# Kernel tuning notes

Hardware: AMD Instinct MI355X
Metric: run time of the kernel (lower is better)

The kernel has to match this reference:

```python
import jax, jax.numpy as jnp
import numpy as np


def _ln(x, w, b):
    m = x.mean(-1, keepdims=True)
    v = ((x - m) ** 2).mean(-1, keepdims=True)
    return (x - m) / jnp.sqrt(v + 1e-5) * w + b


def setup_inputs() -> dict:
    key = jax.random.key(0)
    ks = jax.random.split(key, 8)
    N, C, H, W = 2, 64, 128, 128
    heads, ksz = 2, 7
    C4 = 4 * C
    p = lambda k, shape: jax.random.normal(k, shape, dtype=jnp.float32) * 0.02
    return {
        "x": jax.random.normal(ks[0], (N, C, H, W), dtype=jnp.float32),
        "qkv_w": p(ks[1], (3 * C, C)),
        "qkv_b": jnp.zeros((3 * C,), jnp.float32),
        "proj_w": p(ks[2], (C, C)),
        "proj_b": jnp.zeros((C,), jnp.float32),
        "rpb": p(ks[3], (heads, 2 * ksz - 1, 2 * ksz - 1)),
        "ln1_w": jnp.ones((C,), jnp.float32),
        "ln1_b": jnp.zeros((C,), jnp.float32),
        "ln2_w": jnp.ones((C,), jnp.float32),
        "ln2_b": jnp.zeros((C,), jnp.float32),
        "fc1_w": p(ks[4], (C4, C)),
        "fc1_b": jnp.zeros((C4,), jnp.float32),
        "fc2_w": p(ks[5], (C, C4)),
        "fc2_b": jnp.zeros((C,), jnp.float32),
    }


def reference(x, qkv_w, qkv_b, proj_w, proj_b, rpb, ln1_w, ln1_b, ln2_w, ln2_b,
              fc1_w, fc1_b, fc2_w, fc2_b):
    N, C, H, W = x.shape
    heads = rpb.shape[0]
    ksz = (rpb.shape[1] + 1) // 2  # kernel size from (2k-1) bias table
    dh = C // heads

    xt = x.transpose(0, 2, 3, 1).reshape(N, H * W, C)  # n (h w) c
    shortcut = xt
    xn = _ln(xt, ln1_w, ln1_b).reshape(N, H, W, C)

    # qkv projection -> (3, N, heads, H, W, dh)
    qkv = (xn @ qkv_w.T + qkv_b).reshape(N, H, W, 3, heads, dh)
    qkv = qkv.transpose(3, 0, 4, 1, 2, 5)
    q = qkv[0] * (dh ** -0.5)
    k = qkv[1]
    v = qkv[2]

    # NATTEN neighborhood: window start clamped so every query sees k x k keys
    sh = jnp.clip(jnp.arange(H) - ksz // 2, 0, H - ksz)
    sw = jnp.clip(jnp.arange(W) - ksz // 2, 0, W - ksz)
    rows = sh[:, None] + jnp.arange(ksz)  # (H, k) key row indices
    cols = sw[:, None] + jnp.arange(ksz)  # (W, k) key col indices

    # relative position bias index: (query - key) + (k-1) in [0, 2k-2]
    rel_h = jnp.arange(H)[:, None] - rows + (ksz - 1)  # (H, k)
    rel_w = jnp.arange(W)[:, None] - cols + (ksz - 1)  # (W, k)
    bias = rpb[:, rel_h][:, :, :, rel_w]               # (heads, H, k, W, k)
    bias = bias.transpose(0, 1, 3, 2, 4)               # (heads, H, W, k, k)

    ri = rows[:, None, :, None]  # (H,1,k,1)
    ci = cols[None, :, None, :]  # (1,W,1,k)
    kwin = k[:, :, ri, ci, :]    # (N, heads, H, W, k, k, dh)
    vwin = v[:, :, ri, ci, :]

    scores = jnp.einsum('nzhwd,nzhwijd->nzhwij', q, kwin) + bias[None]
    attn = jax.nn.softmax(scores.reshape(N, heads, H, W, ksz * ksz), axis=-1)
    out = jnp.einsum('nzhwe,nzhwed->nzhwd', attn,
                     vwin.reshape(N, heads, H, W, ksz * ksz, dh))
    out = out.transpose(0, 2, 3, 1, 4).reshape(N, H, W, C) @ proj_w.T + proj_b

    x2 = shortcut + out.reshape(N, H * W, C)
    y = _ln(x2, ln2_w, ln2_b)
    y = jax.nn.gelu(y @ fc1_w.T + fc1_b, approximate=False) @ fc2_w.T + fc2_b
    x3 = x2 + y
    return x3.reshape(N, H, W, C).transpose(0, 3, 1, 2)
```

## Files before the change

kernel.cpp:

```cpp
#include <hip/hip_runtime.h>
#include <math.h>

#define TQ   32768
#define HWSZ 16384
#define CC   64
#define HH   128
#define WW   128
#define C3   192
#define C4   256
#define KS   7

typedef _Float16 half2v __attribute__((ext_vector_type(2)));
typedef _Float16 half4v __attribute__((ext_vector_type(4)));
typedef _Float16 half8v __attribute__((ext_vector_type(8)));
typedef float    f32x4  __attribute__((ext_vector_type(4)));

#define MFMA16(a, b, c) __builtin_amdgcn_mfma_f32_16x16x32_f16((a), (b), (c), 0, 0, 0)

__device__ __forceinline__ float gelu_f(float v) {
    float z = v * (1.59576912f + 0.07135481f * v * v);
    float e = __expf(-z);
    return v * (1.f / (1.f + e));
}

__global__ __launch_bounds__(256) void k_qkvln(const float* __restrict__ x,
        const float* __restrict__ lnw, const float* __restrict__ lnb,
        const float* __restrict__ qw, const float* __restrict__ qb,
        const float* __restrict__ pw, const float* __restrict__ f1w,
        const float* __restrict__ f2w,
        _Float16* __restrict__ qkv16, _Float16* __restrict__ pw16,
        _Float16* __restrict__ f1w16, _Float16* __restrict__ f2w16) {
    __shared__ union {
        struct { __align__(16) _Float16 A[64 * 72]; __align__(16) _Float16 B[192 * 72]; } st;
        __align__(16) _Float16 outb[64 * 200];
    } u;
    __shared__ float ps1[256], ps2[256], m_s[64], r_s[64];
    __shared__ float w_s[64], b_s[64], bias_s[192];
    int tid = threadIdx.x;
    int t0 = blockIdx.x * 64;
    if (tid < 64) { w_s[tid] = lnw[tid]; b_s[tid] = lnb[tid]; }
    if (tid < 192) bias_s[tid] = qb[tid];
    int tok = tid & 63, cq = tid >> 6;
    int t = t0 + tok;
    int n = t >> 14, hw = t & (HWSZ - 1);
    const float* xr = x + ((size_t)n << 20) + hw;
    float v[16];
    float s = 0.f, s2 = 0.f;
#pragma unroll
    for (int e = 0; e < 16; ++e) {
        float f = xr[(cq * 16 + e) * HWSZ];
        v[e] = f; s += f; s2 += f * f;
    }
    ps1[tid] = s; ps2[tid] = s2;
    for (int i = tid; i < 3072; i += 256) {
        int jj = i >> 4, seg = i & 15;
        float4 v4 = *(const float4*)&qw[(size_t)jj * 64 + seg * 4];
        half4v h4 = { (_Float16)v4.x, (_Float16)v4.y, (_Float16)v4.z, (_Float16)v4.w };
        *(half4v*)&u.st.B[jj * 72 + seg * 4] = h4;
    }
    {
        int g = blockIdx.x * 256 + tid;
        if (g < 4096) pw16[g] = (_Float16)pw[g];
        else if (g < 20480) f1w16[g - 4096] = (_Float16)f1w[g - 4096];
        else if (g < 36864) f2w16[g - 20480] = (_Float16)f2w[g - 20480];
    }
    __syncthreads();
    if (tid < 64) {
        float ss = ps1[tid] + ps1[tid + 64] + ps1[tid + 128] + ps1[tid + 192];
        float qq = ps2[tid] + ps2[tid + 64] + ps2[tid + 128] + ps2[tid + 192];
        float m = ss * (1.f / 64.f);
        float var = qq * (1.f / 64.f) - m * m;
        m_s[tid] = m; r_s[tid] = rsqrtf(var + 1e-5f);
    }
    __syncthreads();
    {
        float m = m_s[tok], r = r_s[tok];
#pragma unroll
        for (int u8 = 0; u8 < 2; ++u8) {
            half8v o;
#pragma unroll
            for (int e = 0; e < 8; ++e) {
                int c = cq * 16 + u8 * 8 + e;
                o[e] = (_Float16)((v[u8 * 8 + e] - m) * r * w_s[c] + b_s[c]);
            }
            *(half8v*)&u.st.A[tok * 72 + cq * 16 + u8 * 8] = o;
        }
    }
    __syncthreads();
    int lane = tid & 63, wv = tid >> 6;
    int quad = lane >> 4, l16 = lane & 15;
    int nt0 = wv * 48;
    f32x4 acc[4][3];
#pragma unroll
    for (int mf = 0; mf < 4; ++mf)
#pragma unroll
        for (int nf = 0; nf < 3; ++nf) acc[mf][nf] = (f32x4){0.f, 0.f, 0.f, 0.f};
#pragma unroll
    for (int ks = 0; ks < 64; ks += 32) {
        half8v a[4], bfr[3];
#pragma unroll
        for (int mf = 0; mf < 4; ++mf)
            a[mf] = *(const half8v*)&u.st.A[(mf * 16 + l16) * 72 + ks + quad * 8];
#pragma unroll
        for (int nf = 0; nf < 3; ++nf)
            bfr[nf] = *(const half8v*)&u.st.B[(nt0 + nf * 16 + l16) * 72 + ks + quad * 8];
#pragma unroll
        for (int mf = 0; mf < 4; ++mf)
#pragma unroll
            for (int nf = 0; nf < 3; ++nf) acc[mf][nf] = MFMA16(a[mf], bfr[nf], acc[mf][nf]);
    }
    __syncthreads();
    const float qscale = 0.17677669529663687f;
#pragma unroll
    for (int mf = 0; mf < 4; ++mf)
#pragma unroll
        for (int nf = 0; nf < 3; ++nf) {
            int j = nt0 + nf * 16 + l16;
            float bias = bias_s[j];
            float sc = (j < 64) ? qscale : 1.f;
#pragma unroll
            for (int r = 0; r < 4; ++r) {
                int tl = mf * 16 + quad * 4 + r;
                u.outb[tl * 200 + j] = (_Float16)((acc[mf][nf][r] + bias) * sc);
            }
        }
    __syncthreads();
    for (int i = tid; i < 2048; i += 256) {
        int tk = i >> 5, rem = i & 31;
        if (rem < 24)
            *(half8v*)&qkv16[(size_t)(t0 + tk) * C3 + rem * 8] =
                *(const half8v*)&u.outb[tk * 200 + rem * 8];
    }
}

__global__ __launch_bounds__(256) void k_attn_mlp(const _Float16* __restrict__ qkv16,
        const float* __restrict__ rpb,
        const _Float16* __restrict__ pw16, const float* __restrict__ pb,
        const float* __restrict__ x,
        const float* __restrict__ ln2w, const float* __restrict__ ln2b,
        const _Float16* __restrict__ f1w16, const float* __restrict__ f1b,
        const _Float16* __restrict__ f2w16, const float* __restrict__ f2b,
        float* __restrict__ out) {
    __shared__ __align__(16) char smem[78216];
    _Float16* kv_s  = (_Float16*)smem;
    _Float16* q_s   = (_Float16*)(smem + 53312);
    _Float16* s_s   = (_Float16*)(smem + 63552);
    float*    rpb_s = (float*)(smem + 76352);
    float*    sum_s = (float*)(smem + 77704);
    float* x2t  = (float*)smem;
    float* ps1  = (float*)(smem + 20480);
    float* ps2  = (float*)(smem + 21504);
    float* m_s  = (float*)(smem + 22528);
    float* r_s  = (float*)(smem + 22784);
    float* w_s  = (float*)(smem + 23040);
    float* b_s  = (float*)(smem + 23296);
    float* pb_s = (float*)(smem + 23552);
    _Float16* A2_s = (_Float16*)(smem + 53312);
    _Float16* H_s  = (_Float16*)(smem + 17408);
    float*    tr_s = (float*)(smem + 17408);
    float*    f1b_s = (float*)(smem + 63552);
    float*    f2b_s = (float*)(smem + 64576);

    int tid = threadIdx.x;
    int bx = blockIdx.x;
    int n  = bx >> 8;
    int th = (bx >> 4) & 15, tw = bx & 15;
    int h0 = th * 8, w0 = tw * 8;
    int wr0 = min(max(h0 - 3, 0), HH - 14);
    int ww0 = min(max(w0 - 3, 0), WW - 14);
    int tbase = n << 14;
    int lane = tid & 63, wvi = tid >> 6;
    int quad = lane >> 4, l16 = lane & 15;

    for (int i = tid; i < 338; i += 256) rpb_s[i] = rpb[i];
    for (int i = tid; i < 196 * 16; i += 256) {
        int tok = i >> 4, u = i & 15;
        int wi = tok / 14, wj = tok - wi * 14;
        *(half8v*)&kv_s[tok * 136 + u * 8] = *(const half8v*)&qkv16[
            (size_t)(tbase + (wr0 + wi) * WW + ww0 + wj) * C3 + 64 + u * 8];
    }
    for (int i = tid; i < 64 * 8; i += 256) {
        int q = i >> 3, u = i & 7;
        int qg = tbase + (h0 + (q >> 3)) * WW + (w0 + (q & 7));
        *(half8v*)&q_s[q * 80 + u * 8] = *(const half8v*)&qkv16[(size_t)qg * C3 + u * 8];
    }
    half8v pwr0 = *(const half8v*)&pw16[(size_t)tid * 8];
    half8v pwr1 = *(const half8v*)&pw16[(size_t)(tid + 256) * 8];
    __syncthreads();

    int c16 = tid & 1, z = (tid >> 1) & 1, q = tid >> 2;
    int qy = q >> 3, qx = q & 7;
    int h = h0 + qy, wc = w0 + qx;
    int sh = min(max(h - 3, 0), HH - KS);
    int sw = min(max(wc - 3, 0), WW - KS);
    int oh = sh - wr0, ow = sw - ww0;
    int dhp = h - sh + 6, dwp = wc - sw + 6;
    {
        const half8v* qp = (const half8v*)&q_s[q * 80 + z * 32];
        half8v q0 = qp[0], q1 = qp[1], q2 = qp[2], q3 = qp[3];
        int i7 = 0, j7 = c16;
        for (int nb = c16; nb < 49; nb += 2) {
            int tok = (oh + i7) * 14 + (ow + j7);
            const half8v* kp = (const half8v*)&kv_s[tok * 136 + z * 32];
            half2v acc2 = { (_Float16)0.f, (_Float16)0.f };
            half8v k0 = kp[0], k1 = kp[1], k2 = kp[2], k3 = kp[3];
            acc2 += (half2v){k0.s0, k0.s1} * (half2v){q0.s0, q0.s1};
            acc2 += (half2v){k0.s2, k0.s3} * (half2v){q0.s2, q0.s3};
            acc2 += (half2v){k0.s4, k0.s5} * (half2v){q0.s4, q0.s5};
            acc2 += (half2v){k0.s6, k0.s7} * (half2v){q0.s6, q0.s7};
            acc2 += (half2v){k1.s0, k1.s1} * (half2v){q1.s0, q1.s1};
            acc2 += (half2v){k1.s2, k1.s3} * (half2v){q1.s2, q1.s3};
            acc2 += (half2v){k1.s4, k1.s5} * (half2v){q1.s4, q1.s5};
            acc2 += (half2v){k1.s6, k1.s7} * (half2v){q1.s6, q1.s7};
            acc2 += (half2v){k2.s0, k2.s1} * (half2v){q2.s0, q2.s1};
            acc2 += (half2v){k2.s2, k2.s3} * (half2v){q2.s2, q2.s3};
            acc2 += (half2v){k2.s4, k2.s5} * (half2v){q2.s4, q2.s5};
            acc2 += (half2v){k2.s6, k2.s7} * (half2v){q2.s6, q2.s7};
            acc2 += (half2v){k3.s0, k3.s1} * (half2v){q3.s0, q3.s1};
            acc2 += (half2v){k3.s2, k3.s3} * (half2v){q3.s2, q3.s3};
            acc2 += (half2v){k3.s4, k3.s5} * (half2v){q3.s4, q3.s5};
            acc2 += (half2v){k3.s6, k3.s7} * (half2v){q3.s6, q3.s7};
            float s = (float)acc2.x + (float)acc2.y
                    + rpb_s[(z * 13 + (dhp - i7)) * 13 + (dwp - j7)];
            s_s[(q * 2 + z) * 50 + nb] = (_Float16)s;
            j7 += 2;
            if (j7 >= 7) { j7 -= 7; ++i7; }
        }
    }
    __syncthreads();

    {
        int row = tid >> 1, h2 = tid & 1;
        _Float16* sp = &s_s[row * 50];
        int i0 = h2 ? 25 : 0, i1 = h2 ? 49 : 25;
        float mx = -1e30f;
        for (int i = i0; i < i1; ++i) mx = fmaxf(mx, (float)sp[i]);
        mx = fmaxf(mx, __shfl_xor(mx, 1));
        float sum = 0.f;
        for (int i = i0; i < i1; ++i) {
            float e = __expf((float)sp[i] - mx);
            sum += e;
            sp[i] = (_Float16)e;
        }
        sum += __shfl_xor(sum, 1);
        if (h2 == 0) sum_s[row] = 1.f / sum;
    }
    __syncthreads();

    {
        const _Float16* pp = &s_s[(q * 2 + z) * 50];
        half2v acc[8];
#pragma unroll
        for (int j = 0; j < 8; ++j) acc[j] = (half2v){ (_Float16)0.f, (_Float16)0.f };
        int i7 = 0, j7 = 0;
        for (int nb = 0; nb < 49; ++nb) {
            int tok = (oh + i7) * 14 + (ow + j7);
            _Float16 p = pp[nb];
            half2v p2 = { p, p };
            const half8v* vp = (const half8v*)&kv_s[tok * 136 + 64 + z * 32 + c16 * 16];
            half8v v0 = vp[0], v1 = vp[1];
            acc[0] += (half2v){v0.s0, v0.s1} * p2;
            acc[1] += (half2v){v0.s2, v0.s3} * p2;
            acc[2] += (half2v){v0.s4, v0.s5} * p2;
            acc[3] += (half2v){v0.s6, v0.s7} * p2;
            acc[4] += (half2v){v1.s0, v1.s1} * p2;
            acc[5] += (half2v){v1.s2, v1.s3} * p2;
            acc[6] += (half2v){v1.s4, v1.s5} * p2;
            acc[7] += (half2v){v1.s6, v1.s7} * p2;
            ++j7;
            if (j7 == 7) { j7 = 0; ++i7; }
        }
        float inv = sum_s[q * 2 + z];
        _Float16* op = q_s + q * 72 + z * 32 + c16 * 16;
        half8v o0, o1;
#pragma unroll
        for (int j = 0; j < 4; ++j) {
            o0[2 * j]     = (_Float16)((float)acc[j].x * inv);
            o0[2 * j + 1] = (_Float16)((float)acc[j].y * inv);
            o1[2 * j]     = (_Float16)((float)acc[4 + j].x * inv);
            o1[2 * j + 1] = (_Float16)((float)acc[4 + j].y * inv);
        }
        *(half8v*)op = o0;
        *(half8v*)(op + 8) = o1;
    }
    __syncthreads();
    {
        int i0 = tid, i1 = tid + 256;
        *(half8v*)&s_s[(i0 >> 3) * 72 + (i0 & 7) * 8] = pwr0;
        *(half8v*)&s_s[(i1 >> 3) * 72 + (i1 & 7) * 8] = pwr1;
    }
    if (tid < 64) { w_s[tid] = ln2w[tid]; b_s[tid] = ln2b[tid]; pb_s[tid] = pb[tid]; }
    __syncthreads();
    {
        int mt0 = wvi * 16;
        f32x4 acc2[4];
#pragma unroll
        for (int nf = 0; nf < 4; ++nf) acc2[nf] = (f32x4){0.f, 0.f, 0.f, 0.f};
#pragma unroll
        for (int ks = 0; ks < 64; ks += 32) {
            half8v a = *(const half8v*)&q_s[(mt0 + l16) * 72 + ks + quad * 8];
            half8v bfr[4];
#pragma unroll
            for (int nf = 0; nf < 4; ++nf)
                bfr[nf] = *(const half8v*)&s_s[(nf * 16 + l16) * 72 + ks + quad * 8];
#pragma unroll
            for (int nf = 0; nf < 4; ++nf) acc2[nf] = MFMA16(a, bfr[nf], acc2[nf]);
        }
        __syncthreads();
        int tl0 = mt0 + quad * 4;
        int hwl = (h0 + (tl0 >> 3)) * WW + w0 + (tl0 & 7);
#pragma unroll
        for (int nf = 0; nf < 4; ++nf) {
            int j = nf * 16 + l16;
            float bias = pb_s[j];
            float4 rx = *(const float4*)&x[((size_t)(n * CC + j) << 14) + hwl];
#pragma unroll
            for (int r = 0; r < 4; ++r)
                x2t[(tl0 + r) * 68 + j] = acc2[nf][r] + bias + ((const float*)&rx)[r];
        }
    }
    f1b_s[tid] = f1b[tid];
    if (tid < 64) f2b_s[tid] = f2b[tid];
    __syncthreads();
    int tok = tid & 63, cq = tid >> 6;
    {
        float s = 0.f, s2 = 0.f;
#pragma unroll
        for (int e = 0; e < 16; ++e) {
            float f = x2t[tok * 68 + cq * 16 + e];
            s += f; s2 += f * f;
        }
        ps1[tid] = s; ps2[tid] = s2;
    }
    __syncthreads();
    if (tid < 64) {
        float ss = ps1[tid] + ps1[64 + tid] + ps1[128 + tid] + ps1[192 + tid];
        float qq = ps2[tid] + ps2[64 + tid] + ps2[128 + tid] + ps2[192 + tid];
        float m = ss * (1.f / 64.f);
        float var = qq * (1.f / 64.f) - m * m;
        m_s[tid] = m; r_s[tid] = rsqrtf(var + 1e-5f);
    }
    __syncthreads();
    {
        float m = m_s[tok], r = r_s[tok];
        half8v nv0, nv1;
#pragma unroll
        for (int e = 0; e < 8; ++e) {
            int c = cq * 16 + e;
            float f = x2t[tok * 68 + c];
            nv0[e] = (_Float16)((f - m) * r * w_s[c] + b_s[c]);
        }
#pragma unroll
        for (int e = 0; e < 8; ++e) {
            int c = cq * 16 + 8 + e;
            float f = x2t[tok * 68 + c];
            nv1[e] = (_Float16)((f - m) * r * w_s[c] + b_s[c]);
        }
        *(half8v*)&A2_s[tok * 72 + cq * 16] = nv0;
        *(half8v*)&A2_s[tok * 72 + cq * 16 + 8] = nv1;
    }
    __syncthreads();
    {
        int nt0 = wvi * 64;
        f32x4 acc[4][4];
#pragma unroll
        for (int mf = 0; mf < 4; ++mf)
#pragma unroll
            for (int nf = 0; nf < 4; ++nf) acc[mf][nf] = (f32x4){0.f, 0.f, 0.f, 0.f};
#pragma unroll
        for (int ks = 0; ks < 64; ks += 32) {
            half8v a[4], bfr[4];
#pragma unroll
            for (int mf = 0; mf < 4; ++mf)
                a[mf] = *(const half8v*)&A2_s[(mf * 16 + l16) * 72 + ks + quad * 8];
#pragma unroll
            for (int nf = 0; nf < 4; ++nf)
                bfr[nf] = *(const half8v*)&f1w16[(size_t)(nt0 + nf * 16 + l16) * 64 + ks + quad * 8];
#pragma unroll
            for (int mf = 0; mf < 4; ++mf)
#pragma unroll
                for (int nf = 0; nf < 4; ++nf) acc[mf][nf] = MFMA16(a[mf], bfr[nf], acc[mf][nf]);
        }
#pragma unroll
        for (int mf = 0; mf < 4; ++mf)
#pragma unroll
            for (int nf = 0; nf < 4; ++nf) {
                int jl = nt0 + nf * 16 + l16;
                float bias = f1b_s[jl];
#pragma unroll
                for (int r = 0; r < 4; ++r) {
                    int tl = mf * 16 + quad * 4 + r;
                    H_s[tl * 264 + jl] = (_Float16)gelu_f(acc[mf][nf][r] + bias);
                }
            }
    }
    __syncthreads();
    {
        int mt = wvi * 16;
        f32x4 acc2[4];
#pragma unroll
        for (int nf = 0; nf < 4; ++nf) acc2[nf] = (f32x4){0.f, 0.f, 0.f, 0.f};
#pragma unroll
        for (int ks = 0; ks < 256; ks += 32) {
            half8v a = *(const half8v*)&H_s[(mt + l16) * 264 + ks + quad * 8];
            half8v bfr[4];
#pragma unroll
            for (int nf = 0; nf < 4; ++nf)
                bfr[nf] = *(const half8v*)&f2w16[(size_t)(nf * 16 + l16) * 256 + ks + quad * 8];
#pragma unroll
            for (int nf = 0; nf < 4; ++nf) acc2[nf] = MFMA16(a, bfr[nf], acc2[nf]);
        }
        __syncthreads();
#pragma unroll
        for (int nf = 0; nf < 4; ++nf) {
            int j = nf * 16 + l16;
            float bias = f2b_s[j];
#pragma unroll
            for (int r = 0; r < 4; ++r) {
                int tl = mt + quad * 4 + r;
                float v = acc2[nf][r] + bias + x2t[tl * 68 + j];
                tr_s[j * 68 + tl] = v;
            }
        }
    }
    __syncthreads();
    for (int i = tid; i < 2048; i += 256) {
        int j = i >> 5, tl = (i & 31) * 2;
        *(float2*)&out[((size_t)(n * CC + j) << 14)
                       + (size_t)((h0 + (tl >> 3)) * WW + w0 + (tl & 7))] =
            *(const float2*)&tr_s[j * 68 + tl];
    }
}

extern "C" void kernel_launch(void* const* d_in, const int* in_sizes, int n_in,
                              void* d_out, int out_size, void* d_ws, size_t ws_size,
                              hipStream_t stream) {
    const float* x      = (const float*)d_in[0];
    const float* qkv_w  = (const float*)d_in[1];
    const float* qkv_b  = (const float*)d_in[2];
    const float* proj_w = (const float*)d_in[3];
    const float* proj_b = (const float*)d_in[4];
    const float* rpb    = (const float*)d_in[5];
    const float* ln1_w  = (const float*)d_in[6];
    const float* ln1_b  = (const float*)d_in[7];
    const float* ln2_w  = (const float*)d_in[8];
    const float* ln2_b  = (const float*)d_in[9];
    const float* fc1_w  = (const float*)d_in[10];
    const float* fc1_b  = (const float*)d_in[11];
    const float* fc2_w  = (const float*)d_in[12];
    const float* fc2_b  = (const float*)d_in[13];
    float* out = (float*)d_out;
    char* ws = (char*)d_ws;

    _Float16* qkv16  = (_Float16*)(ws);
    _Float16* pw16   = (_Float16*)(ws + 20971520);
    _Float16* f1w16  = (_Float16*)(ws + 20979712);
    _Float16* f2w16  = (_Float16*)(ws + 21012480);

    k_qkvln   <<<512, 256, 0, stream>>>(x, ln1_w, ln1_b, qkv_w, qkv_b,
                                        proj_w, fc1_w, fc2_w,
                                        qkv16, pw16, f1w16, f2w16);
    k_attn_mlp<<<512, 256, 0, stream>>>(qkv16, rpb, pw16, proj_b, x, ln2_w, ln2_b,
                                        f1w16, fc1_b, f2w16, fc2_b, out);
}
```

Measured before the change: 127.8 us.

## Fuse LN1+QKV projection into attention kernel, recomputing halo tokens per tile

Removes the separate LN1/QKV kernel and its fp16 qkv workspace round-trip. Each 8x8 tile block now loads the 14x14 halo of x directly, applies LayerNorm, and runs the QKV MFMA GEMM in four 49-token chunks, writing K/V and the in-tile Q straight into shared memory. Weights are converted from fp32 to fp16 on the fly instead of being pre-converted. The trade is recomputing QKV for about three times as many tokens as needed (the halo overlap), plus redundant weight conversion in every block, in exchange for one fewer launch and less global traffic.

```diff
diff --git a/kernel.cpp b/kernel.cpp
--- a/kernel.cpp
+++ b/kernel.cpp
@@ -1,13 +1,10 @@
 #include <hip/hip_runtime.h>
 #include <math.h>
 
-#define TQ   32768
 #define HWSZ 16384
 #define CC   64
 #define HH   128
 #define WW   128
-#define C3   192
-#define C4   256
 #define KS   7
 
 typedef _Float16 half2v __attribute__((ext_vector_type(2)));
@@ -23,123 +20,21 @@
     return v * (1.f / (1.f + e));
 }
 
-__global__ __launch_bounds__(256) void k_qkvln(const float* __restrict__ x,
-        const float* __restrict__ lnw, const float* __restrict__ lnb,
-        const float* __restrict__ qw, const float* __restrict__ qb,
-        const float* __restrict__ pw, const float* __restrict__ f1w,
-        const float* __restrict__ f2w,
-        _Float16* __restrict__ qkv16, _Float16* __restrict__ pw16,
-        _Float16* __restrict__ f1w16, _Float16* __restrict__ f2w16) {
-    __shared__ union {
-        struct { __align__(16) _Float16 A[64 * 72]; __align__(16) _Float16 B[192 * 72]; } st;
-        __align__(16) _Float16 outb[64 * 200];
-    } u;
-    __shared__ float ps1[256], ps2[256], m_s[64], r_s[64];
-    __shared__ float w_s[64], b_s[64], bias_s[192];
-    int tid = threadIdx.x;
-    int t0 = blockIdx.x * 64;
-    if (tid < 64) { w_s[tid] = lnw[tid]; b_s[tid] = lnb[tid]; }
-    if (tid < 192) bias_s[tid] = qb[tid];
-    int tok = tid & 63, cq = tid >> 6;
-    int t = t0 + tok;
-    int n = t >> 14, hw = t & (HWSZ - 1);
-    const float* xr = x + ((size_t)n << 20) + hw;
-    float v[16];
-    float s = 0.f, s2 = 0.f;
-#pragma unroll
-    for (int e = 0; e < 16; ++e) {
-        float f = xr[(cq * 16 + e) * HWSZ];
-        v[e] = f; s += f; s2 += f * f;
-    }
-    ps1[tid] = s; ps2[tid] = s2;
-    for (int i = tid; i < 3072; i += 256) {
-        int jj = i >> 4, seg = i & 15;
-        float4 v4 = *(const float4*)&qw[(size_t)jj * 64 + seg * 4];
-        half4v h4 = { (_Float16)v4.x, (_Float16)v4.y, (_Float16)v4.z, (_Float16)v4.w };
-        *(half4v*)&u.st.B[jj * 72 + seg * 4] = h4;
-    }
-    {
-        int g = blockIdx.x * 256 + tid;
-        if (g < 4096) pw16[g] = (_Float16)pw[g];
-        else if (g < 20480) f1w16[g - 4096] = (_Float16)f1w[g - 4096];
-        else if (g < 36864) f2w16[g - 20480] = (_Float16)f2w[g - 20480];
-    }
-    __syncthreads();
-    if (tid < 64) {
-        float ss = ps1[tid] + ps1[tid + 64] + ps1[tid + 128] + ps1[tid + 192];
-        float qq = ps2[tid] + ps2[tid + 64] + ps2[tid + 128] + ps2[tid + 192];
-        float m = ss * (1.f / 64.f);
-        float var = qq * (1.f / 64.f) - m * m;
-        m_s[tid] = m; r_s[tid] = rsqrtf(var + 1e-5f);
-    }
-    __syncthreads();
-    {
-        float m = m_s[tok], r = r_s[tok];
-#pragma unroll
-        for (int u8 = 0; u8 < 2; ++u8) {
-            half8v o;
-#pragma unroll
-            for (int e = 0; e < 8; ++e) {
-                int c = cq * 16 + u8 * 8 + e;
-                o[e] = (_Float16)((v[u8 * 8 + e] - m) * r * w_s[c] + b_s[c]);
-            }
-            *(half8v*)&u.st.A[tok * 72 + cq * 16 + u8 * 8] = o;
-        }
-    }
-    __syncthreads();
-    int lane = tid & 63, wv = tid >> 6;
-    int quad = lane >> 4, l16 = lane & 15;
-    int nt0 = wv * 48;
-    f32x4 acc[4][3];
-#pragma unroll
-    for (int mf = 0; mf < 4; ++mf)
-#pragma unroll
-        for (int nf = 0; nf < 3; ++nf) acc[mf][nf] = (f32x4){0.f, 0.f, 0.f, 0.f};
-#pragma unroll
-    for (int ks = 0; ks < 64; ks += 32) {
-        half8v a[4], bfr[3];
-#pragma unroll
-        for (int mf = 0; mf < 4; ++mf)
-            a[mf] = *(const half8v*)&u.st.A[(mf * 16 + l16) * 72 + ks + quad * 8];
-#pragma unroll
-        for (int nf = 0; nf < 3; ++nf)
-            bfr[nf] = *(const half8v*)&u.st.B[(nt0 + nf * 16 + l16) * 72 + ks + quad * 8];
-#pragma unroll
-        for (int mf = 0; mf < 4; ++mf)
-#pragma unroll
-            for (int nf = 0; nf < 3; ++nf) acc[mf][nf] = MFMA16(a[mf], bfr[nf], acc[mf][nf]);
-    }
-    __syncthreads();
-    const float qscale = 0.17677669529663687f;
-#pragma unroll
-    for (int mf = 0; mf < 4; ++mf)
-#pragma unroll
-        for (int nf = 0; nf < 3; ++nf) {
-            int j = nt0 + nf * 16 + l16;
-            float bias = bias_s[j];
-            float sc = (j < 64) ? qscale : 1.f;
-#pragma unroll
-            for (int r = 0; r < 4; ++r) {
-                int tl = mf * 16 + quad * 4 + r;
-                u.outb[tl * 200 + j] = (_Float16)((acc[mf][nf][r] + bias) * sc);
-            }
-        }
-    __syncthreads();
-    for (int i = tid; i < 2048; i += 256) {
-        int tk = i >> 5, rem = i & 31;
-        if (rem < 24)
-            *(half8v*)&qkv16[(size_t)(t0 + tk) * C3 + rem * 8] =
-                *(const half8v*)&u.outb[tk * 200 + rem * 8];
-    }
+__device__ __forceinline__ half8v cvt8(const float* p) {
+    float4 a0 = *(const float4*)p, a1 = *(const float4*)(p + 4);
+    return (half8v){(_Float16)a0.x, (_Float16)a0.y, (_Float16)a0.z, (_Float16)a0.w,
+                    (_Float16)a1.x, (_Float16)a1.y, (_Float16)a1.z, (_Float16)a1.w};
 }
 
-__global__ __launch_bounds__(256) void k_attn_mlp(const _Float16* __restrict__ qkv16,
+__global__ __launch_bounds__(256) void k_block(
+        const float* __restrict__ x,
+        const float* __restrict__ qw,  const float* __restrict__ qb,
+        const float* __restrict__ pw,  const float* __restrict__ pb,
         const float* __restrict__ rpb,
-        const _Float16* __restrict__ pw16, const float* __restrict__ pb,
-        const float* __restrict__ x,
+        const float* __restrict__ ln1w, const float* __restrict__ ln1b,
         const float* __restrict__ ln2w, const float* __restrict__ ln2b,
-        const _Float16* __restrict__ f1w16, const float* __restrict__ f1b,
-        const _Float16* __restrict__ f2w16, const float* __restrict__ f2b,
+        const float* __restrict__ f1w, const float* __restrict__ f1b,
+        const float* __restrict__ f2w, const float* __restrict__ f2b,
         float* __restrict__ out) {
     __shared__ __align__(16) char smem[78216];
     _Float16* kv_s  = (_Float16*)smem;
@@ -147,6 +42,12 @@
     _Float16* s_s   = (_Float16*)(smem + 63552);
     float*    rpb_s = (float*)(smem + 76352);
     float*    sum_s = (float*)(smem + 77704);
+    _Float16* A_s   = (_Float16*)(smem + 63552);
+    float* ps1c  = (float*)(smem + 72768);
+    float* ps2c  = (float*)(smem + 73184);
+    float* lnw_s = (float*)(smem + 73600);
+    float* lnb_s = (float*)(smem + 73856);
+    float* qb_s  = (float*)(smem + 74112);
     float* x2t  = (float*)smem;
     float* ps1  = (float*)(smem + 20480);
     float* ps2  = (float*)(smem + 21504);
@@ -168,24 +69,112 @@
     int h0 = th * 8, w0 = tw * 8;
     int wr0 = min(max(h0 - 3, 0), HH - 14);
     int ww0 = min(max(w0 - 3, 0), WW - 14);
-    int tbase = n << 14;
     int lane = tid & 63, wvi = tid >> 6;
     int quad = lane >> 4, l16 = lane & 15;
 
+    if (tid < 64) { lnw_s[tid] = ln1w[tid]; lnb_s[tid] = ln1b[tid]; }
+    if (tid < 192) qb_s[tid] = qb[tid];
     for (int i = tid; i < 338; i += 256) rpb_s[i] = rpb[i];
-    for (int i = tid; i < 196 * 16; i += 256) {
-        int tok = i >> 4, u = i & 15;
-        int wi = tok / 14, wj = tok - wi * 14;
-        *(half8v*)&kv_s[tok * 136 + u * 8] = *(const half8v*)&qkv16[
-            (size_t)(tbase + (wr0 + wi) * WW + ww0 + wj) * C3 + 64 + u * 8];
-    }
-    for (int i = tid; i < 64 * 8; i += 256) {
-        int q = i >> 3, u = i & 7;
-        int qg = tbase + (h0 + (q >> 3)) * WW + (w0 + (q & 7));
-        *(half8v*)&q_s[q * 80 + u * 8] = *(const half8v*)&qkv16[(size_t)qg * C3 + u * 8];
-    }
-    half8v pwr0 = *(const half8v*)&pw16[(size_t)tid * 8];
-    half8v pwr1 = *(const half8v*)&pw16[(size_t)(tid + 256) * 8];
+
+    int nt0 = wvi * 48;
+    half8v bq[3][2];
+#pragma unroll
+    for (int nf = 0; nf < 3; ++nf)
+#pragma unroll
+        for (int k2 = 0; k2 < 2; ++k2)
+            bq[nf][k2] = cvt8(&qw[(size_t)(nt0 + nf * 16 + l16) * 64 + k2 * 32 + quad * 8]);
+
+    float4 pr0 = *(const float4*)&pw[tid * 8];
+    float4 pr1 = *(const float4*)&pw[tid * 8 + 4];
+    float4 pr2 = *(const float4*)&pw[2048 + tid * 8];
+    float4 pr3 = *(const float4*)&pw[2048 + tid * 8 + 4];
+
+    {
+        int tkk = tid & 127, hfc = tid >> 7;
+        const float qscale = 0.17677669529663687f;
+        int base_ih = h0 - wr0, base_iw = w0 - ww0;
+        for (int c = 0; c < 4; ++c) {
+            float xv[32]; float s1v = 0.f, s2v = 0.f;
+            if (tkk < 49) {
+                int tok = c * 49 + tkk;
+                int wi = tok / 14, wj = tok - wi * 14;
+                const float* xp = x + (((size_t)(n * CC + hfc * 32)) << 14)
+                                    + (wr0 + wi) * WW + (ww0 + wj);
+#pragma unroll
+                for (int e = 0; e < 32; ++e) {
+                    float f = xp[(size_t)e << 14];
+                    xv[e] = f; s1v += f; s2v += f * f;
+                }
+                ps1c[hfc * 52 + tkk] = s1v; ps2c[hfc * 52 + tkk] = s2v;
+            }
+            __syncthreads();
+            if (tkk < 49) {
+                float ss = ps1c[tkk] + ps1c[52 + tkk];
+                float qq = ps2c[tkk] + ps2c[52 + tkk];
+                float m = ss * (1.f / 64.f);
+                float r = rsqrtf(qq * (1.f / 64.f) - m * m + 1e-5f);
+#pragma unroll
+                for (int u8 = 0; u8 < 4; ++u8) {
+                    half8v o;
+#pragma unroll
+                    for (int e = 0; e < 8; ++e) {
+                        int ch = hfc * 32 + u8 * 8 + e;
+                        o[e] = (_Float16)((xv[u8 * 8 + e] - m) * r * lnw_s[ch] + lnb_s[ch]);
+                    }
+                    *(half8v*)&A_s[tkk * 72 + hfc * 32 + u8 * 8] = o;
+                }
+            }
+            __syncthreads();
+            {
+                f32x4 acc[4][3];
+#pragma unroll
+                for (int mf = 0; mf < 4; ++mf)
+#pragma unroll
+                    for (int nf = 0; nf < 3; ++nf) acc[mf][nf] = (f32x4){0.f, 0.f, 0.f, 0.f};
+#pragma unroll
+                for (int k2 = 0; k2 < 2; ++k2) {
+                    half8v a[4];
+#pragma unroll
+                    for (int mf = 0; mf < 4; ++mf)
+                        a[mf] = *(const half8v*)&A_s[(mf * 16 + l16) * 72 + k2 * 32 + quad * 8];
+#pragma unroll
+                    for (int mf = 0; mf < 4; ++mf)
+#pragma unroll
+                        for (int nf = 0; nf < 3; ++nf)
+                            acc[mf][nf] = MFMA16(a[mf], bq[nf][k2], acc[mf][nf]);
+                }
+#pragma unroll
+                for (int mf = 0; mf < 4; ++mf)
+#pragma unroll
+                    for (int nf = 0; nf < 3; ++nf) {
+                        int j = nt0 + nf * 16 + l16;
+                        float bias = qb_s[j];
+                        if (j >= 64) {
+#pragma unroll
+                            for (int r = 0; r < 4; ++r) {
+                                int tl = mf * 16 + quad * 4 + r;
+                                if (tl < 49)
+                                    kv_s[(c * 49 + tl) * 136 + (j - 64)] =
+                                        (_Float16)(acc[mf][nf][r] + bias);
+                            }
+                        } else {
+#pragma unroll
+                            for (int r = 0; r < 4; ++r) {
+                                int tl = mf * 16 + quad * 4 + r;
+                                if (tl < 49) {
+                                    int tq = c * 49 + tl;
+                                    int qwi = tq / 14, qwj = tq - qwi * 14;
+                                    int ih = qwi - base_ih, iw = qwj - base_iw;
+                                    if ((unsigned)ih < 8u && (unsigned)iw < 8u)
+                                        q_s[(ih * 8 + iw) * 80 + j] =
+                                            (_Float16)((acc[mf][nf][r] + bias) * qscale);
+                                }
+                            }
+                        }
+                    }
+            }
+        }
+    }
     __syncthreads();
 
     int c16 = tid & 1, z = (tid >> 1) & 1, q = tid >> 2;
@@ -285,9 +274,13 @@
     }
     __syncthreads();
     {
-        int i0 = tid, i1 = tid + 256;
-        *(half8v*)&s_s[(i0 >> 3) * 72 + (i0 & 7) * 8] = pwr0;
-        *(half8v*)&s_s[(i1 >> 3) * 72 + (i1 & 7) * 8] = pwr1;
+        int jj = tid >> 3, c8 = tid & 7;
+        half8v w0v = {(_Float16)pr0.x, (_Float16)pr0.y, (_Float16)pr0.z, (_Float16)pr0.w,
+                      (_Float16)pr1.x, (_Float16)pr1.y, (_Float16)pr1.z, (_Float16)pr1.w};
+        half8v w1v = {(_Float16)pr2.x, (_Float16)pr2.y, (_Float16)pr2.z, (_Float16)pr2.w,
+                      (_Float16)pr3.x, (_Float16)pr3.y, (_Float16)pr3.z, (_Float16)pr3.w};
+        *(half8v*)&s_s[jj * 72 + c8 * 8] = w0v;
+        *(half8v*)&s_s[(32 + jj) * 72 + c8 * 8] = w1v;
     }
     if (tid < 64) { w_s[tid] = ln2w[tid]; b_s[tid] = ln2b[tid]; pb_s[tid] = pb[tid]; }
     __syncthreads();
@@ -361,7 +354,7 @@
     }
     __syncthreads();
     {
-        int nt0 = wvi * 64;
+        int nt1 = wvi * 64;
         f32x4 acc[4][4];
 #pragma unroll
         for (int mf = 0; mf < 4; ++mf)
@@ -375,7 +368,7 @@
                 a[mf] = *(const half8v*)&A2_s[(mf * 16 + l16) * 72 + ks + quad * 8];
 #pragma unroll
             for (int nf = 0; nf < 4; ++nf)
-                bfr[nf] = *(const half8v*)&f1w16[(size_t)(nt0 + nf * 16 + l16) * 64 + ks + quad * 8];
+                bfr[nf] = cvt8(&f1w[(size_t)(nt1 + nf * 16 + l16) * 64 + ks + quad * 8]);
 #pragma unroll
             for (int mf = 0; mf < 4; ++mf)
 #pragma unroll
@@ -385,7 +378,7 @@
         for (int mf = 0; mf < 4; ++mf)
 #pragma unroll
             for (int nf = 0; nf < 4; ++nf) {
-                int jl = nt0 + nf * 16 + l16;
+                int jl = nt1 + nf * 16 + l16;
                 float bias = f1b_s[jl];
 #pragma unroll
                 for (int r = 0; r < 4; ++r) {
@@ -406,7 +399,7 @@
             half8v bfr[4];
 #pragma unroll
             for (int nf = 0; nf < 4; ++nf)
-                bfr[nf] = *(const half8v*)&f2w16[(size_t)(nf * 16 + l16) * 256 + ks + quad * 8];
+                bfr[nf] = cvt8(&f2w[(size_t)(nf * 16 + l16) * 256 + ks + quad * 8]);
 #pragma unroll
             for (int nf = 0; nf < 4; ++nf) acc2[nf] = MFMA16(a, bfr[nf], acc2[nf]);
         }
@@ -450,16 +443,9 @@
     const float* fc2_w  = (const float*)d_in[12];
     const float* fc2_b  = (const float*)d_in[13];
     float* out = (float*)d_out;
-    char* ws = (char*)d_ws;
-
-    _Float16* qkv16  = (_Float16*)(ws);
-    _Float16* pw16   = (_Float16*)(ws + 20971520);
-    _Float16* f1w16  = (_Float16*)(ws + 20979712);
-    _Float16* f2w16  = (_Float16*)(ws + 21012480);
-
-    k_qkvln   <<<512, 256, 0, stream>>>(x, ln1_w, ln1_b, qkv_w, qkv_b,
-                                        proj_w, fc1_w, fc2_w,
-                                        qkv16, pw16, f1w16, f2w16);
-    k_attn_mlp<<<512, 256, 0, stream>>>(qkv16, rpb, pw16, proj_b, x, ln2_w, ln2_b,
-                                        f1w16, fc1_b, f2w16, fc2_b, out);
+    (void)d_ws; (void)ws_size;
+
+    k_block<<<512, 256, 0, stream>>>(x, qkv_w, qkv_b, proj_w, proj_b, rpb,
+                                     ln1_w, ln1_b, ln2_w, ln2_b,
+                                     fc1_w, fc1_b, fc2_w, fc2_b, out);
 }
```

After: 172.7 us. 35.1% more time.

## Double threads per block and repartition work in both kernels

Applied to the files above, without the earlier changes.

The LN+QKV kernel now runs 512-thread blocks, each handling 128 tokens, with waves split over both M and N tiles. The fused attention+MLP kernel moves to 512 threads on the same 64-query tile. Each thread's share of QK, softmax, PV, the LayerNorm reductions and the MFMA tiles for proj/fc1/fc2 shrinks to fit. The goal is more waves per CU within the same shared-memory footprint, to better hide latency, at the cost of more synchronization participants and less register-level reuse per wave.

```diff
diff --git a/kernel.cpp b/kernel.cpp
--- a/kernel.cpp
+++ b/kernel.cpp
@@ -23,7 +23,7 @@
     return v * (1.f / (1.f + e));
 }
 
-__global__ __launch_bounds__(256) void k_qkvln(const float* __restrict__ x,
+__global__ __launch_bounds__(512) void k_qkvln(const float* __restrict__ x,
         const float* __restrict__ lnw, const float* __restrict__ lnb,
         const float* __restrict__ qw, const float* __restrict__ qb,
         const float* __restrict__ pw, const float* __restrict__ f1w,
@@ -31,16 +31,16 @@
         _Float16* __restrict__ qkv16, _Float16* __restrict__ pw16,
         _Float16* __restrict__ f1w16, _Float16* __restrict__ f2w16) {
     __shared__ union {
-        struct { __align__(16) _Float16 A[64 * 72]; __align__(16) _Float16 B[192 * 72]; } st;
-        __align__(16) _Float16 outb[64 * 200];
+        struct { __align__(16) _Float16 A[128 * 72]; __align__(16) _Float16 B[192 * 72]; } st;
+        __align__(16) _Float16 outb[128 * 200];
     } u;
-    __shared__ float ps1[256], ps2[256], m_s[64], r_s[64];
+    __shared__ float ps1[512], ps2[512], m_s[128], r_s[128];
     __shared__ float w_s[64], b_s[64], bias_s[192];
     int tid = threadIdx.x;
-    int t0 = blockIdx.x * 64;
+    int t0 = blockIdx.x * 128;
     if (tid < 64) { w_s[tid] = lnw[tid]; b_s[tid] = lnb[tid]; }
     if (tid < 192) bias_s[tid] = qb[tid];
-    int tok = tid & 63, cq = tid >> 6;
+    int tok = tid & 127, cq = tid >> 7;
     int t = t0 + tok;
     int n = t >> 14, hw = t & (HWSZ - 1);
     const float* xr = x + ((size_t)n << 20) + hw;
@@ -52,22 +52,22 @@
         v[e] = f; s += f; s2 += f * f;
     }
     ps1[tid] = s; ps2[tid] = s2;
-    for (int i = tid; i < 3072; i += 256) {
+    for (int i = tid; i < 3072; i += 512) {
         int jj = i >> 4, seg = i & 15;
         float4 v4 = *(const float4*)&qw[(size_t)jj * 64 + seg * 4];
         half4v h4 = { (_Float16)v4.x, (_Float16)v4.y, (_Float16)v4.z, (_Float16)v4.w };
         *(half4v*)&u.st.B[jj * 72 + seg * 4] = h4;
     }
     {
-        int g = blockIdx.x * 256 + tid;
+        int g = blockIdx.x * 512 + tid;
         if (g < 4096) pw16[g] = (_Float16)pw[g];
         else if (g < 20480) f1w16[g - 4096] = (_Float16)f1w[g - 4096];
         else if (g < 36864) f2w16[g - 20480] = (_Float16)f2w[g - 20480];
     }
     __syncthreads();
-    if (tid < 64) {
-        float ss = ps1[tid] + ps1[tid + 64] + ps1[tid + 128] + ps1[tid + 192];
-        float qq = ps2[tid] + ps2[tid + 64] + ps2[tid + 128] + ps2[tid + 192];
+    if (tid < 128) {
+        float ss = ps1[tid] + ps1[tid + 128] + ps1[tid + 256] + ps1[tid + 384];
+        float qq = ps2[tid] + ps2[tid + 128] + ps2[tid + 256] + ps2[tid + 384];
         float m = ss * (1.f / 64.f);
         float var = qq * (1.f / 64.f) - m * m;
         m_s[tid] = m; r_s[tid] = rsqrtf(var + 1e-5f);
@@ -89,7 +89,7 @@
     __syncthreads();
     int lane = tid & 63, wv = tid >> 6;
     int quad = lane >> 4, l16 = lane & 15;
-    int nt0 = wv * 48;
+    int mt0 = (wv & 1) * 64, nt0 = (wv >> 1) * 48;
     f32x4 acc[4][3];
 #pragma unroll
     for (int mf = 0; mf < 4; ++mf)
@@ -100,7 +100,7 @@
         half8v a[4], bfr[3];
 #pragma unroll
         for (int mf = 0; mf < 4; ++mf)
-            a[mf] = *(const half8v*)&u.st.A[(mf * 16 + l16) * 72 + ks + quad * 8];
+            a[mf] = *(const half8v*)&u.st.A[(mt0 + mf * 16 + l16) * 72 + ks + quad * 8];
 #pragma unroll
         for (int nf = 0; nf < 3; ++nf)
             bfr[nf] = *(const half8v*)&u.st.B[(nt0 + nf * 16 + l16) * 72 + ks + quad * 8];
@@ -120,12 +120,12 @@
             float sc = (j < 64) ? qscale : 1.f;
 #pragma unroll
             for (int r = 0; r < 4; ++r) {
-                int tl = mf * 16 + quad * 4 + r;
+                int tl = mt0 + mf * 16 + quad * 4 + r;
                 u.outb[tl * 200 + j] = (_Float16)((acc[mf][nf][r] + bias) * sc);
             }
         }
     __syncthreads();
-    for (int i = tid; i < 2048; i += 256) {
+    for (int i = tid; i < 4096; i += 512) {
         int tk = i >> 5, rem = i & 31;
         if (rem < 24)
             *(half8v*)&qkv16[(size_t)(t0 + tk) * C3 + rem * 8] =
@@ -133,7 +133,7 @@
     }
 }
 
-__global__ __launch_bounds__(256) void k_attn_mlp(const _Float16* __restrict__ qkv16,
+__global__ __launch_bounds__(512, 4) void k_attn_mlp(const _Float16* __restrict__ qkv16,
         const float* __restrict__ rpb,
         const _Float16* __restrict__ pw16, const float* __restrict__ pb,
         const float* __restrict__ x,
@@ -149,12 +149,12 @@
     float*    sum_s = (float*)(smem + 77704);
     float* x2t  = (float*)smem;
     float* ps1  = (float*)(smem + 20480);
-    float* ps2  = (float*)(smem + 21504);
-    float* m_s  = (float*)(smem + 22528);
-    float* r_s  = (float*)(smem + 22784);
-    float* w_s  = (float*)(smem + 23040);
-    float* b_s  = (float*)(smem + 23296);
-    float* pb_s = (float*)(smem + 23552);
+    float* ps2  = (float*)(smem + 22528);
+    float* m_s  = (float*)(smem + 24576);
+    float* r_s  = (float*)(smem + 24832);
+    float* w_s  = (float*)(smem + 25088);
+    float* b_s  = (float*)(smem + 25344);
+    float* pb_s = (float*)(smem + 25600);
     _Float16* A2_s = (_Float16*)(smem + 53312);
     _Float16* H_s  = (_Float16*)(smem + 17408);
     float*    tr_s = (float*)(smem + 17408);
@@ -172,23 +172,22 @@
     int lane = tid & 63, wvi = tid >> 6;
     int quad = lane >> 4, l16 = lane & 15;
 
-    for (int i = tid; i < 338; i += 256) rpb_s[i] = rpb[i];
-    for (int i = tid; i < 196 * 16; i += 256) {
-        int tok = i >> 4, u = i & 15;
-        int wi = tok / 14, wj = tok - wi * 14;
-        *(half8v*)&kv_s[tok * 136 + u * 8] = *(const half8v*)&qkv16[
+    for (int i = tid; i < 338; i += 512) rpb_s[i] = rpb[i];
+    for (int i = tid; i < 196 * 16; i += 512) {
+        int tk = i >> 4, u = i & 15;
+        int wi = tk / 14, wj = tk - wi * 14;
+        *(half8v*)&kv_s[tk * 136 + u * 8] = *(const half8v*)&qkv16[
             (size_t)(tbase + (wr0 + wi) * WW + ww0 + wj) * C3 + 64 + u * 8];
     }
-    for (int i = tid; i < 64 * 8; i += 256) {
-        int q = i >> 3, u = i & 7;
-        int qg = tbase + (h0 + (q >> 3)) * WW + (w0 + (q & 7));
-        *(half8v*)&q_s[q * 80 + u * 8] = *(const half8v*)&qkv16[(size_t)qg * C3 + u * 8];
-    }
-    half8v pwr0 = *(const half8v*)&pw16[(size_t)tid * 8];
-    half8v pwr1 = *(const half8v*)&pw16[(size_t)(tid + 256) * 8];
-    __syncthreads();
-
-    int c16 = tid & 1, z = (tid >> 1) & 1, q = tid >> 2;
+    {
+        int q8 = tid >> 3, u8 = tid & 7;
+        int qg = tbase + (h0 + (q8 >> 3)) * WW + (w0 + (q8 & 7));
+        *(half8v*)&q_s[q8 * 80 + u8 * 8] = *(const half8v*)&qkv16[(size_t)qg * C3 + u8 * 8];
+    }
+    half8v pwr = *(const half8v*)&pw16[(size_t)tid * 8];
+    __syncthreads();
+
+    int p4 = tid & 3, z = (tid >> 2) & 1, q = tid >> 3;
     int qy = q >> 3, qx = q & 7;
     int h = h0 + qy, wc = w0 + qx;
     int sh = min(max(h - 3, 0), HH - KS);
@@ -198,10 +197,10 @@
     {
         const half8v* qp = (const half8v*)&q_s[q * 80 + z * 32];
         half8v q0 = qp[0], q1 = qp[1], q2 = qp[2], q3 = qp[3];
-        int i7 = 0, j7 = c16;
-        for (int nb = c16; nb < 49; nb += 2) {
-            int tok = (oh + i7) * 14 + (ow + j7);
-            const half8v* kp = (const half8v*)&kv_s[tok * 136 + z * 32];
+        int i7 = 0, j7 = p4;
+        for (int nb = p4; nb < 49; nb += 4) {
+            int tk = (oh + i7) * 14 + (ow + j7);
+            const half8v* kp = (const half8v*)&kv_s[tk * 136 + z * 32];
             half2v acc2 = { (_Float16)0.f, (_Float16)0.f };
             half8v k0 = kp[0], k1 = kp[1], k2 = kp[2], k3 = kp[3];
             acc2 += (half2v){k0.s0, k0.s1} * (half2v){q0.s0, q0.s1};
@@ -223,119 +222,111 @@
             float s = (float)acc2.x + (float)acc2.y
                     + rpb_s[(z * 13 + (dhp - i7)) * 13 + (dwp - j7)];
             s_s[(q * 2 + z) * 50 + nb] = (_Float16)s;
-            j7 += 2;
+            j7 += 4;
             if (j7 >= 7) { j7 -= 7; ++i7; }
         }
     }
     __syncthreads();
 
     {
-        int row = tid >> 1, h2 = tid & 1;
+        int row = tid >> 2, h4 = tid & 3;
         _Float16* sp = &s_s[row * 50];
-        int i0 = h2 ? 25 : 0, i1 = h2 ? 49 : 25;
         float mx = -1e30f;
-        for (int i = i0; i < i1; ++i) mx = fmaxf(mx, (float)sp[i]);
+        for (int i = h4; i < 49; i += 4) mx = fmaxf(mx, (float)sp[i]);
         mx = fmaxf(mx, __shfl_xor(mx, 1));
+        mx = fmaxf(mx, __shfl_xor(mx, 2));
         float sum = 0.f;
-        for (int i = i0; i < i1; ++i) {
+        for (int i = h4; i < 49; i += 4) {
             float e = __expf((float)sp[i] - mx);
             sum += e;
             sp[i] = (_Float16)e;
         }
         sum += __shfl_xor(sum, 1);
-        if (h2 == 0) sum_s[row] = 1.f / sum;
-    }
-    __syncthreads();
-
-    {
+        sum += __shfl_xor(sum, 2);
+        if (h4 == 0) sum_s[row] = 1.f / sum;
+    }
+    __syncthreads();
+
+    {
+        int c8 = tid & 3;
         const _Float16* pp = &s_s[(q * 2 + z) * 50];
-        half2v acc[8];
-#pragma unroll
-        for (int j = 0; j < 8; ++j) acc[j] = (half2v){ (_Float16)0.f, (_Float16)0.f };
+        half2v acc[4];
+#pragma unroll
+        for (int j = 0; j < 4; ++j) acc[j] = (half2v){ (_Float16)0.f, (_Float16)0.f };
         int i7 = 0, j7 = 0;
         for (int nb = 0; nb < 49; ++nb) {
-            int tok = (oh + i7) * 14 + (ow + j7);
+            int tk = (oh + i7) * 14 + (ow + j7);
             _Float16 p = pp[nb];
             half2v p2 = { p, p };
-            const half8v* vp = (const half8v*)&kv_s[tok * 136 + 64 + z * 32 + c16 * 16];
-            half8v v0 = vp[0], v1 = vp[1];
+            half8v v0 = *(const half8v*)&kv_s[tk * 136 + 64 + z * 32 + c8 * 8];
             acc[0] += (half2v){v0.s0, v0.s1} * p2;
             acc[1] += (half2v){v0.s2, v0.s3} * p2;
             acc[2] += (half2v){v0.s4, v0.s5} * p2;
             acc[3] += (half2v){v0.s6, v0.s7} * p2;
-            acc[4] += (half2v){v1.s0, v1.s1} * p2;
-            acc[5] += (half2v){v1.s2, v1.s3} * p2;
-            acc[6] += (half2v){v1.s4, v1.s5} * p2;
-            acc[7] += (half2v){v1.s6, v1.s7} * p2;
             ++j7;
             if (j7 == 7) { j7 = 0; ++i7; }
         }
         float inv = sum_s[q * 2 + z];
-        _Float16* op = q_s + q * 72 + z * 32 + c16 * 16;
-        half8v o0, o1;
+        half8v o0;
 #pragma unroll
         for (int j = 0; j < 4; ++j) {
             o0[2 * j]     = (_Float16)((float)acc[j].x * inv);
             o0[2 * j + 1] = (_Float16)((float)acc[j].y * inv);
-            o1[2 * j]     = (_Float16)((float)acc[4 + j].x * inv);
-            o1[2 * j + 1] = (_Float16)((float)acc[4 + j].y * inv);
-        }
-        *(half8v*)op = o0;
-        *(half8v*)(op + 8) = o1;
-    }
-    __syncthreads();
-    {
-        int i0 = tid, i1 = tid + 256;
-        *(half8v*)&s_s[(i0 >> 3) * 72 + (i0 & 7) * 8] = pwr0;
-        *(half8v*)&s_s[(i1 >> 3) * 72 + (i1 & 7) * 8] = pwr1;
-    }
+        }
+        *(half8v*)(q_s + q * 72 + z * 32 + c8 * 8) = o0;
+    }
+    __syncthreads();
+    *(half8v*)&s_s[(tid >> 3) * 72 + (tid & 7) * 8] = pwr;
     if (tid < 64) { w_s[tid] = ln2w[tid]; b_s[tid] = ln2b[tid]; pb_s[tid] = pb[tid]; }
     __syncthreads();
     {
-        int mt0 = wvi * 16;
-        f32x4 acc2[4];
-#pragma unroll
-        for (int nf = 0; nf < 4; ++nf) acc2[nf] = (f32x4){0.f, 0.f, 0.f, 0.f};
+        int mt0 = (wvi & 3) * 16, n0 = (wvi >> 2) * 32;
+        f32x4 acc2[2];
+#pragma unroll
+        for (int nf = 0; nf < 2; ++nf) acc2[nf] = (f32x4){0.f, 0.f, 0.f, 0.f};
 #pragma unroll
         for (int ks = 0; ks < 64; ks += 32) {
             half8v a = *(const half8v*)&q_s[(mt0 + l16) * 72 + ks + quad * 8];
-            half8v bfr[4];
-#pragma unroll
-            for (int nf = 0; nf < 4; ++nf)
-                bfr[nf] = *(const half8v*)&s_s[(nf * 16 + l16) * 72 + ks + quad * 8];
-#pragma unroll
-            for (int nf = 0; nf < 4; ++nf) acc2[nf] = MFMA16(a, bfr[nf], acc2[nf]);
+            half8v bfr[2];
+#pragma unroll
+            for (int nf = 0; nf < 2; ++nf)
+                bfr[nf] = *(const half8v*)&s_s[(n0 + nf * 16 + l16) * 72 + ks + quad * 8];
+#pragma unroll
+            for (int nf = 0; nf < 2; ++nf) acc2[nf] = MFMA16(a, bfr[nf], acc2[nf]);
         }
         __syncthreads();
         int tl0 = mt0 + quad * 4;
         int hwl = (h0 + (tl0 >> 3)) * WW + w0 + (tl0 & 7);
 #pragma unroll
-        for (int nf = 0; nf < 4; ++nf) {
-            int j = nf * 16 + l16;
+        for (int nf = 0; nf < 2; ++nf) {
+            int j = n0 + nf * 16 + l16;
             float bias = pb_s[j];
             float4 rx = *(const float4*)&x[((size_t)(n * CC + j) << 14) + hwl];
 #pragma unroll
+            for (int r = 0; r < 2; ++r);
+#pragma unroll
             for (int r = 0; r < 4; ++r)
                 x2t[(tl0 + r) * 68 + j] = acc2[nf][r] + bias + ((const float*)&rx)[r];
         }
     }
-    f1b_s[tid] = f1b[tid];
-    if (tid < 64) f2b_s[tid] = f2b[tid];
+    if (tid < 256) f1b_s[tid] = f1b[tid];
+    else if (tid < 320) f2b_s[tid - 256] = f2b[tid - 256];
     __syncthreads();
     int tok = tid & 63, cq = tid >> 6;
     {
         float s = 0.f, s2 = 0.f;
 #pragma unroll
-        for (int e = 0; e < 16; ++e) {
-            float f = x2t[tok * 68 + cq * 16 + e];
+        for (int e = 0; e < 8; ++e) {
+            float f = x2t[tok * 68 + cq * 8 + e];
             s += f; s2 += f * f;
         }
         ps1[tid] = s; ps2[tid] = s2;
     }
     __syncthreads();
     if (tid < 64) {
-        float ss = ps1[tid] + ps1[64 + tid] + ps1[128 + tid] + ps1[192 + tid];
-        float qq = ps2[tid] + ps2[64 + tid] + ps2[128 + tid] + ps2[192 + tid];
+        float ss = 0.f, qq = 0.f;
+#pragma unroll
+        for (int k = 0; k < 8; ++k) { ss += ps1[tid + 64 * k]; qq += ps2[tid + 64 * k]; }
         float m = ss * (1.f / 64.f);
         float var = qq * (1.f / 64.f) - m * m;
         m_s[tid] = m; r_s[tid] = rsqrtf(var + 1e-5f);
@@ -343,77 +334,70 @@
     __syncthreads();
     {
         float m = m_s[tok], r = r_s[tok];
-        half8v nv0, nv1;
+        half8v nv0;
 #pragma unroll
         for (int e = 0; e < 8; ++e) {
-            int c = cq * 16 + e;
+            int c = cq * 8 + e;
             float f = x2t[tok * 68 + c];
             nv0[e] = (_Float16)((f - m) * r * w_s[c] + b_s[c]);
         }
-#pragma unroll
-        for (int e = 0; e < 8; ++e) {
-            int c = cq * 16 + 8 + e;
-            float f = x2t[tok * 68 + c];
-            nv1[e] = (_Float16)((f - m) * r * w_s[c] + b_s[c]);
-        }
-        *(half8v*)&A2_s[tok * 72 + cq * 16] = nv0;
-        *(half8v*)&A2_s[tok * 72 + cq * 16 + 8] = nv1;
-    }
-    __syncthreads();
-    {
-        int nt0 = wvi * 64;
-        f32x4 acc[4][4];
-#pragma unroll
-        for (int mf = 0; mf < 4; ++mf)
+        *(half8v*)&A2_s[tok * 72 + cq * 8] = nv0;
+    }
+    __syncthreads();
+    {
+        int mt0 = (wvi & 1) * 32, nt1 = (wvi >> 1) * 64;
+        f32x4 acc[2][4];
+#pragma unroll
+        for (int mf = 0; mf < 2; ++mf)
 #pragma unroll
             for (int nf = 0; nf < 4; ++nf) acc[mf][nf] = (f32x4){0.f, 0.f, 0.f, 0.f};
 #pragma unroll
         for (int ks = 0; ks < 64; ks += 32) {
-            half8v a[4], bfr[4];
-#pragma unroll
-            for (int mf = 0; mf < 4; ++mf)
-                a[mf] = *(const half8v*)&A2_s[(mf * 16 + l16) * 72 + ks + quad * 8];
+            half8v a[2], bfr[4];
+#pragma unroll
+            for (int mf = 0; mf < 2; ++mf)
+                a[mf] = *(const half8v*)&A2_s[(mt0 + mf * 16 + l16) * 72 + ks + quad * 8];
 #pragma unroll
             for (int nf = 0; nf < 4; ++nf)
-                bfr[nf] = *(const half8v*)&f1w16[(size_t)(nt0 + nf * 16 + l16) * 64 + ks + quad * 8];
-#pragma unroll
-            for (int mf = 0; mf < 4; ++mf)
+                bfr[nf] = *(const half8v*)&f1w16[(size_t)(nt1 + nf * 16 + l16) * 64 + ks + quad * 8];
+#pragma unroll
+            for (int mf = 0; mf < 2; ++mf)
 #pragma unroll
                 for (int nf = 0; nf < 4; ++nf) acc[mf][nf] = MFMA16(a[mf], bfr[nf], acc[mf][nf]);
         }
 #pragma unroll
-        for (int mf = 0; mf < 4; ++mf)
+        for (int mf = 0; mf < 2; ++mf)
 #pragma unroll
             for (int nf = 0; nf < 4; ++nf) {
-                int jl = nt0 + nf * 16 + l16;
+                int jl = nt1 + nf * 16 + l16;
                 float bias = f1b_s[jl];
 #pragma unroll
                 for (int r = 0; r < 4; ++r) {
-                    int tl = mf * 16 + quad * 4 + r;
+                    int tl = mt0 + mf * 16 + quad * 4 + r;
                     H_s[tl * 264 + jl] = (_Float16)gelu_f(acc[mf][nf][r] + bias);
                 }
             }
     }
     __syncthreads();
     {
-        int mt = wvi * 16;
-        f32x4 acc2[4];
-#pragma unroll
-        for (int nf = 0; nf < 4; ++nf) acc2[nf] = (f32x4){0.f, 0.f, 0.f, 0.f};
+        int mt = (wvi & 3) * 16, n0 = (wvi >> 2) * 32;
+        f32x4 acc2[2];
+#pragma unroll
+        for (int nf = 0; nf < 2; ++nf) acc2[nf] = (f32x4){0.f, 0.f, 0.f, 0.f};
 #pragma unroll
         for (int ks = 0; ks < 256; ks += 32) {
             half8v a = *(const half8v*)&H_s[(mt + l16) * 264 + ks + quad * 8];
-            half8v bfr[4];
-#pragma unroll
-            for (int nf = 0; nf < 4; ++nf)
-                bfr[nf] = *(const half8v*)&f2w16[(size_t)(nf * 16 + l16) * 256 + ks + quad * 8];
-#pragma unroll
-            for (int nf = 0; nf < 4; ++nf) acc2[nf] = MFMA16(a, bfr[nf], acc2[nf]);
+            half8v bfr[2];
+#pragma unroll
+            for (int nf = 0; nf < 2; ++nf)
+                bfr[nf] = *(const half8v*)&f2w16[(size_t)(n0 + nf * 16 + l16) * 256 + ks + quad * 8];
+#pragma unroll
+            for (int nf = 0; nf < 2; ++nf) acc2[nf] = MFMA16(a, bfr[nf], acc2[nf]);
         }
         __syncthreads();
 #pragma unroll
-        for (int nf = 0; nf < 4; ++nf) {
-            int j = nf * 16 + l16;
+        for (int nf = 0; nf < 2; ++nf) {
+            int j = n0 + nf * 16 + l16;
             float bias = f2b_s[j];
 #pragma unroll
             for (int r = 0; r < 4; ++r) {
@@ -424,7 +408,7 @@
         }
     }
     __syncthreads();
-    for (int i = tid; i < 2048; i += 256) {
+    for (int i = tid; i < 2048; i += 512) {
         int j = i >> 5, tl = (i & 31) * 2;
         *(float2*)&out[((size_t)(n * CC + j) << 14)
                        + (size_t)((h0 + (tl >> 3)) * WW + w0 + (tl & 7))] =
@@ -457,9 +441,9 @@
     _Float16* f1w16  = (_Float16*)(ws + 20979712);
     _Float16* f2w16  = (_Float16*)(ws + 21012480);
 
-    k_qkvln   <<<512, 256, 0, stream>>>(x, ln1_w, ln1_b, qkv_w, qkv_b,
+    k_qkvln   <<<256, 512, 0, stream>>>(x, ln1_w, ln1_b, qkv_w, qkv_b,
                                         proj_w, fc1_w, fc2_w,
                                         qkv16, pw16, f1w16, f2w16);
-    k_attn_mlp<<<512, 256, 0, stream>>>(qkv16, rpb, pw16, proj_b, x, ln2_w, ln2_b,
+    k_attn_mlp<<<512, 512, 0, stream>>>(qkv16, rpb, pw16, proj_b, x, ln2_w, ln2_b,
                                         f1w16, fc1_b, f2w16, fc2_b, out);
 }
```

Measured after the change: 124.2 us. 2.8% less time.
